# Performance work log

Hardware: AMD Instinct MI355X
Metric: run time of the kernel (lower is better)

Reference implementation:

```python
import jax, jax.numpy as jnp
import numpy as np

D_MODEL = 1024
NUM_HEADS = 16
HEAD_DIM = D_MODEL // NUM_HEADS


def setup_inputs() -> dict:
    key = jax.random.key(0)
    ks = jax.random.split(key, 10)
    B, SQ, SK = 2, 2048, 2048
    scale = 1.0 / np.sqrt(D_MODEL)
    inp = {
        "x1": jax.random.normal(ks[0], (B, SQ, D_MODEL), jnp.float32),
        "x2": jax.random.normal(ks[1], (B, SK, D_MODEL), jnp.float32),
        "Wq": jax.random.normal(ks[2], (D_MODEL, D_MODEL), jnp.float32) * scale,
        "bq": jnp.zeros((D_MODEL,), jnp.float32),
        "Wk": jax.random.normal(ks[3], (D_MODEL, D_MODEL), jnp.float32) * scale,
        "bk": jnp.zeros((D_MODEL,), jnp.float32),
        "Wv": jax.random.normal(ks[4], (D_MODEL, D_MODEL), jnp.float32) * scale,
        "bv": jnp.zeros((D_MODEL,), jnp.float32),
        "Wo": jax.random.normal(ks[5], (D_MODEL, D_MODEL), jnp.float32) * scale,
        "bo": jnp.zeros((D_MODEL,), jnp.float32),
    }
    return inp


def reference(x1, x2, Wq, bq, Wk, bk, Wv, bv, Wo, bo):
    B, SQ, _ = x1.shape
    SK = x2.shape[1]
    # projections, then split into heads: [B, H, S, Dh]
    def split_heads(t, S):
        return t.reshape(B, S, NUM_HEADS, HEAD_DIM).transpose(0, 2, 1, 3)
    Q = split_heads(x1 @ Wq + bq, SQ)
    K = split_heads(x2 @ Wk + bk, SK)
    V = split_heads(x2 @ Wv + bv, SK)
    # note: original scales by 1/head_dim**0.5
    scores = jnp.einsum("bhqd,bhkd->bhqk", Q, K) / jnp.sqrt(
        jnp.asarray(HEAD_DIM, Q.dtype))
    attn = jax.nn.softmax(scores, axis=-1)
    ctx = jnp.einsum("bhqk,bhkd->bhqd", attn, V)
    ctx = ctx.transpose(0, 2, 1, 3).reshape(B, SQ, D_MODEL)
    return ctx @ Wo + bo
```

## Files before the change

kernel.cpp:

```cpp
#include <hip/hip_runtime.h>
#include <stdint.h>


typedef unsigned short u16b;
typedef __attribute__((ext_vector_type(4))) short short4v;
typedef __attribute__((ext_vector_type(8))) short short8v;
typedef __attribute__((ext_vector_type(4))) float float4v;
typedef __attribute__((ext_vector_type(16))) float float16v;
typedef __attribute__((ext_vector_type(2))) unsigned int uint2v;

#if __has_builtin(__builtin_amdgcn_exp2f)
__device__ __forceinline__ float exp2_fast(float x){ return __builtin_amdgcn_exp2f(x); }
#else
__device__ __forceinline__ float exp2_fast(float x){ return exp2f(x); }
#endif

__device__ __forceinline__ u16b f2bf(float f) {
  union { float f; unsigned int i; } v; v.f = f;
  return (u16b)((v.i + 0x7fffu + ((v.i >> 16) & 1u)) >> 16);
}
__device__ __forceinline__ void gl_lds16(const u16b* g, u16b* l) {
  __builtin_amdgcn_global_load_lds(
      (const __attribute__((address_space(1))) void*)g,
      (__attribute__((address_space(3))) void*)l, 16, 0, 0);
}

#define FENCE_BARRIER() do { asm volatile("" ::: "memory"); \
  __builtin_amdgcn_s_barrier(); asm volatile("" ::: "memory"); } while(0)
#define LGKM0() do { asm volatile("s_waitcnt lgkmcnt(0)" ::: "memory"); \
  __builtin_amdgcn_sched_barrier(0); } while(0)
#define VMCNT(n) do { asm volatile("s_waitcnt vmcnt(" #n ")" ::: "memory"); \
  __builtin_amdgcn_sched_barrier(0); } while(0)

__global__ __launch_bounds__(256) void prep(
    const float* __restrict__ x1, const float* __restrict__ x2,
    const float* __restrict__ W0, const float* __restrict__ W1,
    const float* __restrict__ W2, const float* __restrict__ W3,
    u16b* __restrict__ x1b, u16b* __restrict__ x2b, u16b* __restrict__ WT) {
  const int tid = threadIdx.x;
  const int mode = blockIdx.y;
  if (mode < 2) {
    const float* src = mode ? x2 : x1;
    u16b* dst = mode ? x2b : x1b;
    const int n4 = 1024*1024;
    int i = blockIdx.x * 256 + tid;
    const int stride = gridDim.x * 256;
    for (; i < n4; i += stride) {
      float4v v = ((const float4v*)src)[i];
      short4v o;
      o[0]=(short)f2bf(v[0]); o[1]=(short)f2bf(v[1]);
      o[2]=(short)f2bf(v[2]); o[3]=(short)f2bf(v[3]);
      ((short4v*)dst)[i] = o;
    }
  } else {
    __shared__ u16b tile[32][33];
    const int z = mode - 2;
    const float* src = (z==0) ? W0 : (z==1) ? W1 : (z==2) ? W2 : W3;
    u16b* dst = WT + (size_t)z * (1024*1024);
    const int x = tid & 31, y = tid >> 5;
    const int bx = (blockIdx.x & 31) * 32, by = (blockIdx.x >> 5) * 32;
#pragma unroll
    for (int j=0;j<4;++j)
      tile[y*4+j][x] = f2bf(src[(size_t)(by + y*4+j)*1024 + bx + x]);
    __syncthreads();
#pragma unroll
    for (int j=0;j<4;++j)
      dst[(size_t)(bx + y*4+j)*1024 + by + x] = tile[x][y*4+j];
  }
}

template<bool BIAS_ROW>
__device__ __forceinline__ void gemm256_core(
    u16b* __restrict__ As, u16b* __restrict__ Bs,
    const u16b* __restrict__ A, const u16b* __restrict__ Bt,
    const float* __restrict__ bias, u16b* __restrict__ C,
    int N, int K, int bm, int bn, float oscale) {
  constexpr int ASTR = 256*64, BSTR = 256*64;
  const int tid = threadIdx.x;
  const int lane = tid & 63, wave = tid >> 6;
  const int wr = wave >> 2, wc = wave & 3;
  const int l15 = lane & 15, l4 = lane >> 4;

  auto stage_half = [&](const u16b* __restrict__ G, int row0, int k0,
                        u16b* __restrict__ Lbase) {
#pragma unroll
    for (int j=0;j<2;++j) {
      int idx = j*512 + tid;
      int row = idx >> 3, seg = idx & 7;
      int segg = seg ^ (row & 7);
      gl_lds16(&G[(size_t)(row0+row)*K + k0 + segg*8], &Lbase[idx*8]);
    }
  };

  float4v acc[2][2][4][2];
#pragma unroll
  for (int qm=0;qm<2;++qm)
#pragma unroll
  for (int qn=0;qn<2;++qn)
#pragma unroll
  for (int m=0;m<4;++m)
#pragma unroll
  for (int n=0;n<2;++n) acc[qm][qn][m][n] = (float4v){0.f,0.f,0.f,0.f};

  const int NK = K >> 6;
  stage_half(A,  bm+0,   0,  As + 0);
  stage_half(Bt, bn+0,   0,  Bs + 0);
  stage_half(A,  bm+128, 0,  As + 128*64);
  stage_half(Bt, bn+128, 0,  Bs + 128*64);
  stage_half(A,  bm+0,   64, As + ASTR);
  stage_half(Bt, bn+0,   64, Bs + BSTR);
  VMCNT(4);
  FENCE_BARRIER();

  int cur = 0;
  for (int t = 0; t < NK; ++t) {
    u16b* Ac = As + cur*ASTR;  u16b* Bc = Bs + cur*BSTR;
    u16b* An = As + (cur^1)*ASTR;  u16b* Bn = Bs + (cur^1)*BSTR;
    const int k1 = (t+1) << 6, k2 = (t+2) << 6;
    short8v af[4][2], bf0[2][2], bf1[2][2];

#pragma unroll
    for (int m=0;m<4;++m)
#pragma unroll
      for (int ks=0;ks<2;++ks)
        af[m][ks] = *(const short8v*)&Ac[(0*128 + wr*64 + m*16 + l15)*64
                                         + (((ks*4+l4) ^ (l15&7))*8)];
#pragma unroll
    for (int n=0;n<2;++n)
#pragma unroll
      for (int ks=0;ks<2;++ks)
        bf0[n][ks] = *(const short8v*)&Bc[(0*128 + wc*32 + n*16 + l15)*64
                                          + (((ks*4+l4) ^ (l15&7))*8)];
    if (t+1 < NK) stage_half(A, bm+128, k1, An + 128*64);
    FENCE_BARRIER();
    LGKM0();
    __builtin_amdgcn_s_setprio(1);
#pragma unroll
    for (int m=0;m<4;++m)
#pragma unroll
      for (int n=0;n<2;++n)
#pragma unroll
        for (int ks=0;ks<2;++ks)
          acc[0][0][m][n] = __builtin_amdgcn_mfma_f32_16x16x32_bf16(
              af[m][ks], bf0[n][ks], acc[0][0][m][n], 0, 0, 0);
    __builtin_amdgcn_s_setprio(0);
    FENCE_BARRIER();

#pragma unroll
    for (int n=0;n<2;++n)
#pragma unroll
      for (int ks=0;ks<2;++ks)
        bf1[n][ks] = *(const short8v*)&Bc[(1*128 + wc*32 + n*16 + l15)*64
                                          + (((ks*4+l4) ^ (l15&7))*8)];
    if (t+1 < NK) stage_half(Bt, bn+128, k1, Bn + 128*64);
    FENCE_BARRIER();
    LGKM0();
    __builtin_amdgcn_s_setprio(1);
#pragma unroll
    for (int m=0;m<4;++m)
#pragma unroll
      for (int n=0;n<2;++n)
#pragma unroll
        for (int ks=0;ks<2;++ks)
          acc[0][1][m][n] = __builtin_amdgcn_mfma_f32_16x16x32_bf16(
              af[m][ks], bf1[n][ks], acc[0][1][m][n], 0, 0, 0);
    __builtin_amdgcn_s_setprio(0);
    FENCE_BARRIER();

#pragma unroll
    for (int m=0;m<4;++m)
#pragma unroll
      for (int ks=0;ks<2;++ks)
        af[m][ks] = *(const short8v*)&Ac[(1*128 + wr*64 + m*16 + l15)*64
                                         + (((ks*4+l4) ^ (l15&7))*8)];
    if (t+2 < NK) stage_half(A, bm+0, k2, Ac + 0);
    FENCE_BARRIER();
    LGKM0();
    __builtin_amdgcn_s_setprio(1);
#pragma unroll
    for (int m=0;m<4;++m)
#pragma unroll
      for (int n=0;n<2;++n)
#pragma unroll
        for (int ks=0;ks<2;++ks)
          acc[1][0][m][n] = __builtin_amdgcn_mfma_f32_16x16x32_bf16(
              af[m][ks], bf0[n][ks], acc[1][0][m][n], 0, 0, 0);
    __builtin_amdgcn_s_setprio(0);
    FENCE_BARRIER();

    if (t+2 < NK) stage_half(Bt, bn+0, k2, Bc + 0);
    FENCE_BARRIER();
    LGKM0();
    __builtin_amdgcn_s_setprio(1);
#pragma unroll
    for (int m=0;m<4;++m)
#pragma unroll
      for (int n=0;n<2;++n)
#pragma unroll
        for (int ks=0;ks<2;++ks)
          acc[1][1][m][n] = __builtin_amdgcn_mfma_f32_16x16x32_bf16(
              af[m][ks], bf1[n][ks], acc[1][1][m][n], 0, 0, 0);
    __builtin_amdgcn_s_setprio(0);
    if (t == NK-2) { VMCNT(0); }
    else          { VMCNT(4); }
    FENCE_BARRIER();
    cur ^= 1;
  }

#pragma unroll
  for (int qm=0;qm<2;++qm)
#pragma unroll
  for (int qn=0;qn<2;++qn)
#pragma unroll
  for (int n=0;n<2;++n) {
    int col = bn + qn*128 + wc*32 + n*16 + l15;
    float bbc = BIAS_ROW ? 0.f : bias[col];
#pragma unroll
    for (int m=0;m<4;++m) {
      int row0 = bm + qm*128 + wr*64 + m*16 + l4*4;
#pragma unroll
      for (int r=0;r<4;++r) {
        float bb = BIAS_ROW ? bias[row0+r] : bbc;
        float v = (acc[qm][qn][m][n][r] + bb) * oscale;
        C[(size_t)(row0+r)*N + col] = f2bf(v);
      }
    }
  }
}

__global__ __launch_bounds__(512, 2) void gemm_qkv256(
    const u16b* __restrict__ x1b, const u16b* __restrict__ x2b,
    const u16b* __restrict__ WT, const float* __restrict__ bq,
    const float* __restrict__ bk, const float* __restrict__ bv,
    u16b* __restrict__ QKV) {
  __shared__ __align__(16) u16b As[2*256*64];
  __shared__ __align__(16) u16b Bs[2*256*64];
  const int f = blockIdx.x;
  const int z = f >> 6;
  const int u = f & 63;
  const int w = ((u & 7) << 3) | (u >> 3);
  const size_t Mi = 1024*1024;
  const float QSCALE = 0.125f * 1.4426950408889634f;
  if (z == 2) {
    int bm = (w >> 4) * 256;
    int bn = (w & 15) * 256;
    gemm256_core<true>(As, Bs, WT + 2*Mi, x2b, bv, QKV + 8*Mi,
                       4096, 1024, bm, bn, 1.0f);
  } else {
    int bm = (w >> 2) * 256;
    int bn = (w & 3) * 256;
    gemm256_core<false>(As, Bs, z ? x2b : x1b, WT + (size_t)z*Mi,
                        z ? bk : bq, QKV + (size_t)z*4*Mi,
                        1024, 1024, bm, bn, z ? 1.0f : QSCALE);
  }
}

template<int BN, bool OUT_F32, bool BIAS_ROW>
__device__ __forceinline__ void gemm_core(
    u16b* __restrict__ As, u16b* __restrict__ Bs,
    const u16b* __restrict__ A, const u16b* __restrict__ Bt,
    const float* __restrict__ bias, void* __restrict__ Cv,
    int N, int K, int bm, int bn, float oscale) {
  constexpr int NT = BN / 32;
  constexpr int ASTRIDE = 128*64;
  constexpr int BSTRIDE = BN*64;
  const int tid = threadIdx.x;
  const int lane = tid & 63, wave = tid >> 6;
  const int wm = wave >> 1, wn = wave & 1;
  const int l15 = lane & 15, l4 = lane >> 4;
  float4v acc[4][NT];
#pragma unroll
  for (int i=0;i<4;++i)
#pragma unroll
    for (int j=0;j<NT;++j) acc[i][j] = (float4v){0.f,0.f,0.f,0.f};

  auto stage = [&](int buf, int k0) {
#pragma unroll
    for (int j=0;j<4;++j) {
      int idx = j*256 + tid;
      int row = idx >> 3, seg = idx & 7;
      int segg = seg ^ (row & 7);
      gl_lds16(&A[(size_t)(bm+row)*K + k0 + segg*8], &As[buf*ASTRIDE + idx*8]);
    }
#pragma unroll
    for (int j=0;j<BN/32;++j) {
      int idx = j*256 + tid;
      int row = idx >> 3, seg = idx & 7;
      int segg = seg ^ (row & 7);
      gl_lds16(&Bt[(size_t)(bn+row)*K + k0 + segg*8], &Bs[buf*BSTRIDE + idx*8]);
    }
  };

  const int NK = K >> 6;
  stage(0, 0);
  __syncthreads();
  for (int kt = 0; kt < NK; ++kt) {
    const int cur = kt & 1;
    if (kt + 1 < NK) stage(cur ^ 1, (kt + 1) << 6);
    const u16b* Asb = As + cur*ASTRIDE;
    const u16b* Bsb = Bs + cur*BSTRIDE;
#pragma unroll
    for (int ks=0; ks<2; ++ks) {
      short8v af[4], bf[NT];
      const int cs = ((ks*4 + l4) ^ (l15 & 7)) * 8;
#pragma unroll
      for (int mt=0;mt<4;++mt)
        af[mt] = *(const short8v*)&Asb[(wm*64+mt*16+l15)*64 + cs];
#pragma unroll
      for (int nt=0;nt<NT;++nt)
        bf[nt] = *(const short8v*)&Bsb[(wn*(BN/2)+nt*16+l15)*64 + cs];
#pragma unroll
      for (int mt=0;mt<4;++mt)
#pragma unroll
        for (int nt=0;nt<NT;++nt)
          acc[mt][nt] = __builtin_amdgcn_mfma_f32_16x16x32_bf16(af[mt], bf[nt], acc[mt][nt], 0, 0, 0);
    }
    __syncthreads();
  }

#pragma unroll
  for (int nt=0;nt<NT;++nt) {
    int col = bn + wn*(BN/2) + nt*16 + l15;
    float bbc = BIAS_ROW ? 0.f : bias[col];
#pragma unroll
    for (int mt=0;mt<4;++mt) {
      int row0 = bm + wm*64 + mt*16 + l4*4;
#pragma unroll
      for (int r=0;r<4;++r) {
        float bb = BIAS_ROW ? bias[row0+r] : bbc;
        float v = (acc[mt][nt][r] + bb) * oscale;
        if (OUT_F32) ((float*)Cv)[(size_t)(row0+r)*N + col] = v;
        else         ((u16b*)Cv)[(size_t)(row0+r)*N + col] = f2bf(v);
      }
    }
  }
}

__global__ __launch_bounds__(256) void gemm_out(
    const u16b* __restrict__ A, const u16b* __restrict__ Bt,
    const float* __restrict__ bias, float* __restrict__ C) {
  __shared__ __align__(16) u16b As[2*128*64];
  __shared__ __align__(16) u16b Bs[2*64*64];
  const int f = blockIdx.x;
  const int xcd = f & 7, s = f >> 3;
  const int bm = (xcd*4 + (s >> 4)) * 128;
  const int bn = (s & 15) * 64;
  gemm_core<64,true,false>(As, Bs, A, Bt, bias, C, 1024, 1024, bm, bn, 1.0f);
}

__device__ __forceinline__ void attn_load(
    const u16b* __restrict__ Kgb, const u16b* __restrict__ Vtb,
    int kvoff, int tid, short8v kreg[4], short8v vreg[4]) {
#pragma unroll
  for (int j=0; j<4; ++j) {
    int idx = j*256 + tid;
    int rowk = idx >> 3, segk = idx & 7;
    kreg[j] = *(const short8v*)&Kgb[(size_t)(kvoff+rowk)*1024 + ((segk ^ (rowk & 7))*8)];
    int rowv = idx & 63, segv = idx >> 6;
    vreg[j] = *(const short8v*)&Vtb[(size_t)rowv*4096 + kvoff + segv*8];
  }
}

__global__ __launch_bounds__(256, 2) void attn_q128(
    const u16b* __restrict__ Q, const u16b* __restrict__ Kg,
    const u16b* __restrict__ Vt, u16b* __restrict__ O) {
  __shared__ __align__(16) u16b Ks[128*64];
  __shared__ __align__(16) u16b Vs[64*132];
  const int tid = threadIdx.x;
  const int lane = tid & 63, wave = tid >> 6;
  const int l31 = lane & 31, hi = lane >> 5;
  const int bh = blockIdx.x;
  const int b = bh >> 4, h = bh & 15;
  const int q0 = blockIdx.y * 128;
  const size_t seqbase = (size_t)b * 2048;
  const int colh = h * 64;
  const u16b* Kgb = Kg + seqbase*1024 + colh;
  const u16b* Vtb = Vt + (size_t)(h*64)*4096 + (size_t)b*2048;

  short8v kreg[4], vreg[4];
  attn_load(Kgb, Vtb, 0, tid, kreg, vreg);

  short8v qf[4];
  {
    size_t qrow = seqbase + q0 + wave*32 + l31;
#pragma unroll
    for (int ks=0; ks<4; ++ks)
      qf[ks] = *(const short8v*)&Q[qrow*1024 + colh + ks*16 + hi*8];
  }

  float16v oacc[2];
#pragma unroll
  for (int nb=0; nb<2; ++nb)
#pragma unroll
    for (int r=0; r<16; ++r) oacc[nb][r] = 0.f;
  float lsum = 0.f;

  for (int kt = 0; kt < 16; ++kt) {
    __syncthreads();
#pragma unroll
    for (int j=0; j<4; ++j) {
      int idx = j*256 + tid;
      *(short8v*)&Ks[idx*8] = kreg[j];
      int rowv = idx & 63, segv = idx >> 6;
      union { short8v s; uint2v u[2]; } tv; tv.s = vreg[j];
      *(uint2v*)&Vs[rowv*132 + segv*8]     = tv.u[0];
      *(uint2v*)&Vs[rowv*132 + segv*8 + 4] = tv.u[1];
    }
    __syncthreads();
    if (kt < 15)
      attn_load(Kgb, Vtb, (kt+1)*128, tid, kreg, vreg);

    float16v sacc[4];
#pragma unroll
    for (int kb=0; kb<4; ++kb)
#pragma unroll
      for (int r=0; r<16; ++r) sacc[kb][r] = 0.f;
    __builtin_amdgcn_s_setprio(1);
#pragma unroll
    for (int kb=0; kb<4; ++kb)
#pragma unroll
      for (int ks=0; ks<4; ++ks) {
        int row = kb*32 + l31;
        short8v kf = *(const short8v*)&Ks[row*64 + (((ks*2+hi) ^ (row & 7))*8)];
        sacc[kb] = __builtin_amdgcn_mfma_f32_32x32x16_bf16(kf, qf[ks], sacc[kb], 0, 0, 0);
      }
    __builtin_amdgcn_s_setprio(0);

#pragma unroll
    for (int kb=0; kb<4; ++kb) {
      float e[16];
#pragma unroll
      for (int r=0; r<16; ++r) e[r] = exp2_fast(sacc[kb][r]);
#pragma unroll
      for (int r=0; r<16; ++r) lsum += e[r];
      unsigned int d[8];
#pragma unroll
      for (int i=0; i<8; ++i)
        d[i] = __builtin_amdgcn_perm(__float_as_uint(e[2*i+1]),
                                     __float_as_uint(e[2*i]), 0x07060302u);
      __builtin_amdgcn_s_setprio(1);
#pragma unroll
      for (int s=0; s<4; ++s) {
        union { unsigned int u[2]; short4v s4; } pu;
        pu.u[0] = d[2*s]; pu.u[1] = d[2*s+1];
        const short4v pf = pu.s4;
#pragma unroll
        for (int nb=0; nb<2; ++nb) {
          int row = nb*32 + l31;
          short4v vf = *(const short4v*)&Vs[row*132 + kb*32 + s*8 + hi*4];
          oacc[nb] = __builtin_amdgcn_mfma_f32_32x32x8bf16_1k(pf, vf, oacc[nb], 0, 0, 0);
        }
      }
      __builtin_amdgcn_s_setprio(0);
    }
  }

  float ltot = lsum + __shfl_xor(lsum, 32, 64);
#pragma unroll
  for (int r=0; r<16; ++r) {
    int qloc = (r & 3) + 8*(r >> 2) + 4*hi;
    float lv = __shfl(ltot, qloc, 64);
    float inv = 1.0f / lv;
    size_t row = seqbase + q0 + wave*32 + qloc;
    O[row*1024 + colh +      l31] = f2bf(oacc[0][r] * inv);
    O[row*1024 + colh + 32 + l31] = f2bf(oacc[1][r] * inv);
  }
}

extern "C" void kernel_launch(void* const* d_in, const int* in_sizes, int n_in,
                              void* d_out, int out_size, void* d_ws, size_t ws_size,
                              hipStream_t stream) {
  const float* x1 = (const float*)d_in[0];
  const float* x2 = (const float*)d_in[1];
  const float* Wq = (const float*)d_in[2];
  const float* bq = (const float*)d_in[3];
  const float* Wk = (const float*)d_in[4];
  const float* bk = (const float*)d_in[5];
  const float* Wv = (const float*)d_in[6];
  const float* bv = (const float*)d_in[7];
  const float* Wo = (const float*)d_in[8];
  const float* bo = (const float*)d_in[9];
  (void)in_sizes; (void)n_in; (void)out_size; (void)ws_size;

  u16b* ws = (u16b*)d_ws;
  const size_t Mi = 1024*1024;
  u16b* WT  = ws;
  u16b* WoT = ws + 3*Mi;
  u16b* x1b = ws + 4*Mi;
  u16b* x2b = ws + 8*Mi;
  u16b* QKV = ws + 12*Mi;
  u16b* Qb  = QKV;
  u16b* Kb  = QKV + 4*Mi;
  u16b* Vtb = QKV + 8*Mi;
  u16b* Cx  = x1b;

  prep<<<dim3(1024,6), 256, 0, stream>>>(x1, x2, Wq, Wk, Wv, Wo, x1b, x2b, WT);

  gemm_qkv256<<<dim3(192), 512, 0, stream>>>(x1b, x2b, WT, bq, bk, bv, QKV);

  attn_q128<<<dim3(32,16), 256, 0, stream>>>(Qb, Kb, Vtb, Cx);

  gemm_out<<<dim3(512), 256, 0, stream>>>(Cx, WoT, bo, (float*)d_out);
}
```

Baseline: 202.9 us.

## Double-buffer K/V LDS tiles and use 32x32x16 MFMA for PV

Splits the K and V shared-memory tiles into two buffers. The prefetched next tile is written to the alternate buffer after compute, which drops one __syncthreads per iteration and lets the global loads overlap the MFMA work. It also packs the P fragments into 8-element vectors so the PV product uses the 32x32x16 bf16 MFMA, halving the MFMA instruction count for that step. The cost is double the LDS footprint (about 66KB), which may limit occupancy at 2 blocks per CU.

```diff
diff --git a/kernel.cpp b/kernel.cpp
--- a/kernel.cpp
+++ b/kernel.cpp
@@ -364,8 +364,8 @@
 __global__ __launch_bounds__(256, 2) void attn_q128(
     const u16b* __restrict__ Q, const u16b* __restrict__ Kg,
     const u16b* __restrict__ Vt, u16b* __restrict__ O) {
-  __shared__ __align__(16) u16b Ks[128*64];
-  __shared__ __align__(16) u16b Vs[64*132];
+  __shared__ __align__(16) u16b Ks[2][128*64];
+  __shared__ __align__(16) u16b Vs[2][64*132];
   const int tid = threadIdx.x;
   const int lane = tid & 63, wave = tid >> 6;
   const int l31 = lane & 31, hi = lane >> 5;
@@ -395,20 +395,25 @@
     for (int r=0; r<16; ++r) oacc[nb][r] = 0.f;
   float lsum = 0.f;
 
-  for (int kt = 0; kt < 16; ++kt) {
-    __syncthreads();
+  {
+    u16b* Kw = Ks[0]; u16b* Vw = Vs[0];
 #pragma unroll
     for (int j=0; j<4; ++j) {
       int idx = j*256 + tid;
-      *(short8v*)&Ks[idx*8] = kreg[j];
+      *(short8v*)&Kw[idx*8] = kreg[j];
       int rowv = idx & 63, segv = idx >> 6;
       union { short8v s; uint2v u[2]; } tv; tv.s = vreg[j];
-      *(uint2v*)&Vs[rowv*132 + segv*8]     = tv.u[0];
-      *(uint2v*)&Vs[rowv*132 + segv*8 + 4] = tv.u[1];
-    }
+      *(uint2v*)&Vw[rowv*132 + segv*8]     = tv.u[0];
+      *(uint2v*)&Vw[rowv*132 + segv*8 + 4] = tv.u[1];
+    }
+  }
+
+  for (int kt = 0; kt < 16; ++kt) {
     __syncthreads();
     if (kt < 15)
       attn_load(Kgb, Vtb, (kt+1)*128, tid, kreg, vreg);
+    const u16b* Kb_ = Ks[kt & 1];
+    const u16b* Vb_ = Vs[kt & 1];
 
     float16v sacc[4];
 #pragma unroll
@@ -421,7 +426,7 @@
 #pragma unroll
       for (int ks=0; ks<4; ++ks) {
         int row = kb*32 + l31;
-        short8v kf = *(const short8v*)&Ks[row*64 + (((ks*2+hi) ^ (row & 7))*8)];
+        short8v kf = *(const short8v*)&Kb_[row*64 + (((ks*2+hi) ^ (row & 7))*8)];
         sacc[kb] = __builtin_amdgcn_mfma_f32_32x32x16_bf16(kf, qf[ks], sacc[kb], 0, 0, 0);
       }
     __builtin_amdgcn_s_setprio(0);
@@ -438,20 +443,36 @@
       for (int i=0; i<8; ++i)
         d[i] = __builtin_amdgcn_perm(__float_as_uint(e[2*i+1]),
                                      __float_as_uint(e[2*i]), 0x07060302u);
+      union { unsigned int u[4]; short8v s; } pa0, pa1;
+      pa0.u[0]=d[0]; pa0.u[1]=d[1]; pa0.u[2]=d[2]; pa0.u[3]=d[3];
+      pa1.u[0]=d[4]; pa1.u[1]=d[5]; pa1.u[2]=d[6]; pa1.u[3]=d[7];
       __builtin_amdgcn_s_setprio(1);
 #pragma unroll
-      for (int s=0; s<4; ++s) {
-        union { unsigned int u[2]; short4v s4; } pu;
-        pu.u[0] = d[2*s]; pu.u[1] = d[2*s+1];
-        const short4v pf = pu.s4;
-#pragma unroll
-        for (int nb=0; nb<2; ++nb) {
-          int row = nb*32 + l31;
-          short4v vf = *(const short4v*)&Vs[row*132 + kb*32 + s*8 + hi*4];
-          oacc[nb] = __builtin_amdgcn_mfma_f32_32x32x8bf16_1k(pf, vf, oacc[nb], 0, 0, 0);
-        }
+      for (int nb=0; nb<2; ++nb) {
+        int row = nb*32 + l31;
+        const u16b* vb = &Vb_[row*132 + kb*32 + hi*4];
+        union { short4v h[2]; short8v s; } v0, v1;
+        v0.h[0] = *(const short4v*)(vb);
+        v0.h[1] = *(const short4v*)(vb + 8);
+        v1.h[0] = *(const short4v*)(vb + 16);
+        v1.h[1] = *(const short4v*)(vb + 24);
+        oacc[nb] = __builtin_amdgcn_mfma_f32_32x32x16_bf16(pa0.s, v0.s, oacc[nb], 0, 0, 0);
+        oacc[nb] = __builtin_amdgcn_mfma_f32_32x32x16_bf16(pa1.s, v1.s, oacc[nb], 0, 0, 0);
       }
       __builtin_amdgcn_s_setprio(0);
+    }
+
+    if (kt < 15) {
+      u16b* Kw = Ks[(kt+1) & 1]; u16b* Vw = Vs[(kt+1) & 1];
+#pragma unroll
+      for (int j=0; j<4; ++j) {
+        int idx = j*256 + tid;
+        *(short8v*)&Kw[idx*8] = kreg[j];
+        int rowv = idx & 63, segv = idx >> 6;
+        union { short8v s; uint2v u[2]; } tv; tv.s = vreg[j];
+        *(uint2v*)&Vw[rowv*132 + segv*8]     = tv.u[0];
+        *(uint2v*)&Vw[rowv*132 + segv*8 + 4] = tv.u[1];
+      }
     }
   }
 
```

After: 197.4 us. 1.03x faster.
